# Optimization experiments

Measured on AMD Instinct MI355X. Metric: run time of the kernel, lower is better.

The kernel has to match this reference:

```python
import jax, jax.numpy as jnp
import numpy as np

KS, STRIDE, DIL = 5, 1, 1
PAD = (KS + (KS - 1) * (DIL - 1) - 1) // 2
EPS = 1e-5


def _unfold_t(x):
    # x: (N, C, T, V) -> (N, C, T_out, KS, V), zero-padded temporal windows
    N, C, T, V = x.shape
    xp = jnp.pad(x, ((0, 0), (0, 0), (PAD, PAD), (0, 0)))
    t_out = (T + 2 * PAD - DIL * (KS - 1) - 1) // STRIDE + 1
    idx = jnp.arange(t_out)[:, None] * STRIDE + jnp.arange(KS)[None, :] * DIL  # (T_out, KS)
    return xp[:, :, idx, :]


def _bn2d(x, g, b):
    # training-mode BatchNorm2d: biased batch stats over (N, T, V)
    mu = jnp.mean(x, axis=(0, 2, 3), keepdims=True)
    var = jnp.var(x, axis=(0, 2, 3), keepdims=True)
    xn = (x - mu) * jax.lax.rsqrt(var + EPS)
    return xn * g[None, :, None, None] + b[None, :, None, None]


def setup_inputs() -> dict:
    key = jax.random.key(0)
    ks = jax.random.split(key, 8)
    N, C, T, V = 64, 64, 128, 25
    R, O = 8, 128
    s = 0.05
    return {
        "x": jax.random.normal(ks[0], (N, C, T, V), jnp.float32),
        "Wv": jax.random.normal(ks[1], (R, C), jnp.float32) * s,
        "bv": jax.random.normal(ks[2], (R,), jnp.float32) * s,
        "Ww": jax.random.normal(ks[3], (KS * KS, KS), jnp.float32) * s,
        "bw": jax.random.normal(ks[4], (KS * KS,), jnp.float32) * s,
        "g_bn": jnp.ones((R,), jnp.float32),
        "b_bn": jnp.zeros((R,), jnp.float32),
        "Wr": jax.random.normal(ks[5], (R, C), jnp.float32) * s,
        "br": jax.random.normal(ks[6], (R,), jnp.float32) * s,
        "g_r": jnp.ones((R,), jnp.float32),
        "b_r": jnp.zeros((R,), jnp.float32),
        "Wo": jax.random.normal(ks[7], (O, R), jnp.float32) * s,
        "bo": jnp.zeros((O,), jnp.float32),
        "g_o": jnp.ones((O,), jnp.float32),
        "b_o": jnp.zeros((O,), jnp.float32),
    }


def reference(x, Wv, bv, Ww, bw, g_bn, b_bn, Wr, br, g_r, b_r, Wo, bo, g_o, b_o):
    N, C, T, V = x.shape
    # convV (1x1) then unfold both x and v
    v0 = jnp.einsum('rc,nctv->nrtv', Wv, x) + bv[None, :, None, None]
    xu = _unfold_t(x)      # (N, C, T, W, V)
    vu = _unfold_t(v0)     # (N, R, T, W, V)
    # mean over channels, move window dim to channel position for convW
    m = jnp.mean(xu, axis=1).transpose(0, 2, 1, 3)  # (N, W, T, V)
    w = jnp.einsum('ow,nwtv->notv', Ww, m) + bw[None, :, None, None]
    weights = jnp.tanh(w.reshape(N, KS, KS, T, V))  # (N, W, W, T, V)
    att = jnp.einsum('nwutv,nctuv->nctv', weights, vu)  # (N, R, T, V)
    # residual 1x1 conv + BN (in_channels != out_channels -> conv path)
    res = _bn2d(jnp.einsum('rc,nctv->nrtv', Wr, x) + br[None, :, None, None], g_r, b_r)
    h = _bn2d(att, g_bn, b_bn) + res
    h = jnp.where(h >= 0, h, 0.1 * h)  # LeakyReLU(0.1)
    out = _bn2d(jnp.einsum('or,nrtv->notv', Wo, h) + bo[None, :, None, None], g_o, b_o)
    return out
```

## Files before the change

### kernel.cpp

```cpp
#include <hip/hip_runtime.h>
#include <math.h>

#define TV 3200
#define NTV 204800
#define NB1 512
#define NB2 400
constexpr float EPSF = 1e-5f;

typedef float f2 __attribute__((ext_vector_type(2)));

__device__ inline float fast_tanh(float x){
  float e = __expf(2.f*x);
  return 1.f - 2.f/(e + 1.f);
}

template<int NS>
__device__ inline void write_partials4(float (&vals)[NS], float* __restrict__ outp, int nb, float* lds){
  __syncthreads();
  int lane = threadIdx.x & 63, wid = threadIdx.x >> 6;
  #pragma unroll
  for (int s = 0; s < NS; ++s){
    float v = vals[s];
    #pragma unroll
    for (int o = 32; o > 0; o >>= 1) v += __shfl_down(v, o);
    if (lane == 0) lds[s*4 + wid] = v;
  }
  __syncthreads();
  if ((int)threadIdx.x < NS)
    outp[threadIdx.x*nb + blockIdx.x] = lds[threadIdx.x*4+0] + lds[threadIdx.x*4+1]
                                      + lds[threadIdx.x*4+2] + lds[threadIdx.x*4+3];
}

__global__ __launch_bounds__(256) void k_pw(
    const float* __restrict__ x,
    const float* __restrict__ Wv, const float* __restrict__ bv,
    const float* __restrict__ Wr, const float* __restrict__ br,
    const float* __restrict__ Ww, const float* __restrict__ bw,
    float* __restrict__ r0, float* __restrict__ att,
    float* __restrict__ pr, float* __restrict__ patt)
{
  __shared__ float sV[500*9];
  __shared__ float sS[500];
  __shared__ float sWv[512], sWr[512], sWw[125], sbw[25];
  __shared__ float red[16*4];
  const int tid = threadIdx.x;
  const int b = blockIdx.x, n = b >> 3, q = b & 7;
  const int t0 = q*16;
  for (int i2 = tid; i2 < 512; i2 += 256){ sWv[i2] = Wv[i2]; sWr[i2] = Wr[i2]; }
  if (tid < 125) sWw[tid] = Ww[tid];
  if (tid < 25)  sbw[tid] = bw[tid];
  __syncthreads();

  const int i = tid;
  const bool act = (i < 250);
  const int s0 = 2*i, s1 = 2*i + 1;
  const bool val0 = act && (q > 0 || s0 >= 50) && (q < 7 || s0 < 450);
  const bool val1 = act && (q > 0 || s1 >= 50) && (q < 7 || s1 < 450);
  const bool own  = (i >= 25) && (i < 225);
  const float* xpn = x + (size_t)n*64*TV + (t0*25 - 50);

  float av0[8]={0,0,0,0,0,0,0,0}, av1[8]={0,0,0,0,0,0,0,0};
  float ar0[8]={0,0,0,0,0,0,0,0}, ar1[8]={0,0,0,0,0,0,0,0};
  float ss0 = 0.f, ss1 = 0.f;
  if (val0 && val1){
    #pragma unroll 8
    for (int c = 0; c < 64; ++c){
      f2 xv = *(const f2*)(xpn + (size_t)c*TV + s0);
      ss0 += xv.x; ss1 += xv.y;
      #pragma unroll
      for (int r = 0; r < 8; ++r){
        float wv = sWv[r*64+c], wr = sWr[r*64+c];
        av0[r] = fmaf(wv, xv.x, av0[r]); av1[r] = fmaf(wv, xv.y, av1[r]);
        ar0[r] = fmaf(wr, xv.x, ar0[r]); ar1[r] = fmaf(wr, xv.y, ar1[r]);
      }
    }
  } else if (val0 || val1){
    #pragma unroll 4
    for (int c = 0; c < 64; ++c){
      float x0 = 0.f, x1 = 0.f;
      if (val0) x0 = xpn[(size_t)c*TV + s0];
      if (val1) x1 = xpn[(size_t)c*TV + s1];
      ss0 += x0; ss1 += x1;
      #pragma unroll
      for (int r = 0; r < 8; ++r){
        float wv = sWv[r*64+c], wr = sWr[r*64+c];
        av0[r] = fmaf(wv, x0, av0[r]); av1[r] = fmaf(wv, x1, av1[r]);
        ar0[r] = fmaf(wr, x0, ar0[r]); ar1[r] = fmaf(wr, x1, ar1[r]);
      }
    }
  }
  if (act){
    sS[s0] = ss0 * 0.015625f;
    sS[s1] = ss1 * 0.015625f;
    #pragma unroll
    for (int r = 0; r < 8; ++r){
      float bvr = bv[r];
      sV[s0*9+r] = val0 ? (av0[r] + bvr) : 0.f;
      sV[s1*9+r] = val1 ? (av1[r] + bvr) : 0.f;
    }
  }
  const int gbase = t0*25 - 50 + s0;
  float vals[16];
  {
    float rr0[8], rr1[8];
    if (own){
      float* rp = r0 + (size_t)n*8*TV + gbase;
      #pragma unroll
      for (int r = 0; r < 8; ++r){
        float brr = br[r];
        rr0[r] = ar0[r] + brr; rr1[r] = ar1[r] + brr;
        f2 rv; rv.x = rr0[r]; rv.y = rr1[r];
        *(f2*)(rp + (size_t)r*TV) = rv;
      }
    }
    #pragma unroll
    for (int r = 0; r < 8; ++r){
      vals[r]   = own ? (rr0[r] + rr1[r]) : 0.f;
      vals[8+r] = own ? (rr0[r]*rr0[r] + rr1[r]*rr1[r]) : 0.f;
    }
  }
  write_partials4<16>(vals, pr, NB1, red);

  float at0[8]={0,0,0,0,0,0,0,0}, at1[8]={0,0,0,0,0,0,0,0};
  if (own){
    #pragma unroll
    for (int sl = 0; sl < 2; ++sl){
      int s = s0 + sl;
      float m[5];
      #pragma unroll
      for (int k = 0; k < 5; ++k) m[k] = sS[s + (k-2)*25];
      float w2[5] = {0.f,0.f,0.f,0.f,0.f};
      #pragma unroll
      for (int w = 0; w < 5; ++w){
        #pragma unroll
        for (int u = 0; u < 5; ++u){
          int o = w*5 + u;
          float wo = sbw[o];
          #pragma unroll
          for (int k = 0; k < 5; ++k) wo = fmaf(sWw[o*5+k], m[k], wo);
          w2[u] += fast_tanh(wo);
        }
      }
      float* at = sl ? at1 : at0;
      #pragma unroll
      for (int u = 0; u < 5; ++u){
        float wu = w2[u];
        int base = (s + (u-2)*25)*9;
        #pragma unroll
        for (int r = 0; r < 8; ++r) at[r] = fmaf(wu, sV[base + r], at[r]);
      }
    }
    float* ap = att + (size_t)n*8*TV + gbase;
    #pragma unroll
    for (int r = 0; r < 8; ++r){
      f2 av; av.x = at0[r]; av.y = at1[r];
      *(f2*)(ap + (size_t)r*TV) = av;
    }
  }
  #pragma unroll
  for (int r = 0; r < 8; ++r){
    vals[r]   = own ? (at0[r] + at1[r]) : 0.f;
    vals[8+r] = own ? (at0[r]*at0[r] + at1[r]*at1[r]) : 0.f;
  }
  write_partials4<16>(vals, patt, NB1, red);
}

__global__ __launch_bounds__(256) void k_h(
    const float* __restrict__ att, const float* __restrict__ r0,
    const float* __restrict__ pr, const float* __restrict__ patt,
    const float* __restrict__ g_bn, const float* __restrict__ b_bn,
    const float* __restrict__ g_r, const float* __restrict__ b_r,
    float* __restrict__ h, float* __restrict__ ph)
{
  __shared__ float red[44*4];
  __shared__ float sc[32];
  const int tid = threadIdx.x;
  {
    int g = tid >> 3, l8 = tid & 7;
    const float* src = (g < 16) ? (pr + g*NB1) : (patt + (g-16)*NB1);
    float sm = 0.f;
    for (int k2 = l8; k2 < NB1; k2 += 8) sm += src[k2];
    sm += __shfl_down(sm, 4, 8); sm += __shfl_down(sm, 2, 8); sm += __shfl_down(sm, 1, 8);
    if (l8 == 0) red[g] = sm;
  }
  __syncthreads();
  if (tid < 8){
    int r = tid;
    float mu_r  = red[r]    / (float)NTV;
    float var_r = red[8+r]  / (float)NTV - mu_r*mu_r;
    float ar_ = g_r[r] * rsqrtf(var_r + EPSF);
    sc[16+r] = ar_; sc[24+r] = b_r[r] - ar_*mu_r;
    float mu_a  = red[16+r] / (float)NTV;
    float var_a = red[24+r] / (float)NTV - mu_a*mu_a;
    float aa = g_bn[r] * rsqrtf(var_a + EPSF);
    sc[r] = aa; sc[8+r] = b_bn[r] - aa*mu_a;
  }
  __syncthreads();

  int p = blockIdx.x*256 + tid;
  int n = p / 1600, j = p - n*1600;
  const float* ap = att + (size_t)n*8*TV + 2*j;
  const float* rp = r0  + (size_t)n*8*TV + 2*j;
  float* hp = h + (size_t)n*8*TV + 2*j;
  float h0[8], h1[8];
  #pragma unroll
  for (int r = 0; r < 8; ++r){
    float ca = sc[r], cc = sc[8+r], cr = sc[16+r], cd = sc[24+r];
    f2 a = *(const f2*)(ap + (size_t)r*TV);
    f2 rr = *(const f2*)(rp + (size_t)r*TV);
    float z0 = ca*a.x + cc + cr*rr.x + cd;
    float z1 = ca*a.y + cc + cr*rr.y + cd;
    h0[r] = (z0 >= 0.f) ? z0 : 0.1f*z0;
    h1[r] = (z1 >= 0.f) ? z1 : 0.1f*z1;
    f2 hh; hh.x = h0[r]; hh.y = h1[r];
    *(f2*)(hp + (size_t)r*TV) = hh;
  }
  float vals[44];
  #pragma unroll
  for (int r = 0; r < 8; ++r) vals[r] = h0[r] + h1[r];
  int cnt = 8;
  #pragma unroll
  for (int r = 0; r < 8; ++r){
    #pragma unroll
    for (int r2 = r; r2 < 8; ++r2) vals[cnt++] = h0[r]*h0[r2] + h1[r]*h1[r2];
  }
  write_partials4<44>(vals, ph, NB2, red);
}

__global__ __launch_bounds__(256) void k_out(
    const float* __restrict__ h, const float* __restrict__ ph,
    const float* __restrict__ Wo, const float* __restrict__ bo,
    const float* __restrict__ g_o, const float* __restrict__ b_o,
    float* __restrict__ out)
{
  __shared__ float hstat[44];
  __shared__ float sW[1024], sB[128];
  const int tid = threadIdx.x;
  {
    int lane = tid & 63, wid = tid >> 6;
    for (int s2 = wid; s2 < 44; s2 += 4){
      float sm = 0.f;
      for (int k2 = lane; k2 < NB2; k2 += 64) sm += ph[s2*NB2 + k2];
      #pragma unroll
      for (int o = 32; o > 0; o >>= 1) sm += __shfl_down(sm, o);
      if (lane == 0) hstat[s2] = sm;
    }
  }
  __syncthreads();
  if (tid < 128){
    int o = tid;
    double muh[8];
    #pragma unroll
    for (int r = 0; r < 8; ++r) muh[r] = (double)hstat[r] / (double)NTV;
    double w[8];
    #pragma unroll
    for (int r = 0; r < 8; ++r) w[r] = (double)Wo[o*8+r];
    double bob = (double)bo[o];
    double mu = bob;
    #pragma unroll
    for (int r = 0; r < 8; ++r) mu += w[r]*muh[r];
    double t = 0.0;
    for (int r = 0; r < 8; ++r){
      for (int r2 = 0; r2 < 8; ++r2){
        int lo = (r < r2) ? r : r2, hi = (r < r2) ? r2 : r;
        int idx = 8 + lo*8 - (lo*(lo-1))/2 + (hi - lo);
        t += w[r]*w[r2]*((double)hstat[idx] / (double)NTV);
      }
    }
    double ey2 = t + 2.0*bob*(mu - bob) + bob*bob;
    double var = ey2 - mu*mu;
    double a = (double)g_o[o] / sqrt(var + (double)EPSF);
    #pragma unroll
    for (int r = 0; r < 8; ++r) sW[o*8+r] = (float)(a * w[r]);
    sB[o] = (float)(a * (bob - mu) + (double)b_o[o]);
  }
  __syncthreads();

  int p = blockIdx.x*256 + tid;
  int n = p / 1600, j = p - n*1600;
  const float* hp = h + (size_t)n*8*TV + 2*j;
  float h0[8], h1[8];
  #pragma unroll
  for (int r = 0; r < 8; ++r){
    f2 v = *(const f2*)(hp + (size_t)r*TV);
    h0[r] = v.x; h1[r] = v.y;
  }
  float* op = out + (size_t)n*128*TV + 2*j;
  #pragma unroll 8
  for (int o = 0; o < 128; ++o){
    float y0 = sB[o], y1 = y0;
    #pragma unroll
    for (int r = 0; r < 8; ++r){
      float w = sW[o*8+r];
      y0 = fmaf(w, h0[r], y0); y1 = fmaf(w, h1[r], y1);
    }
    f2 yy; yy.x = y0; yy.y = y1;
    __builtin_nontemporal_store(yy, (f2*)(op + (size_t)o*TV));
  }
}

extern "C" void kernel_launch(void* const* d_in, const int* in_sizes, int n_in,
                              void* d_out, int out_size, void* d_ws, size_t ws_size,
                              hipStream_t stream){
  const float* x    = (const float*)d_in[0];
  const float* Wv   = (const float*)d_in[1];
  const float* bv   = (const float*)d_in[2];
  const float* Ww   = (const float*)d_in[3];
  const float* bw   = (const float*)d_in[4];
  const float* g_bn = (const float*)d_in[5];
  const float* b_bn = (const float*)d_in[6];
  const float* Wr   = (const float*)d_in[7];
  const float* br   = (const float*)d_in[8];
  const float* g_r  = (const float*)d_in[9];
  const float* b_r  = (const float*)d_in[10];
  const float* Wo   = (const float*)d_in[11];
  const float* bo   = (const float*)d_in[12];
  const float* g_o  = (const float*)d_in[13];
  const float* b_o  = (const float*)d_in[14];

  float* ws = (float*)d_ws;
  size_t off = 0;
  float* r0   = ws + off; off += 1638400;
  float* att  = ws + off; off += 1638400;
  float* hbuf = ws + off; off += 1638400;
  float* pr   = ws + off; off += 16*NB1;
  float* patt = ws + off; off += 16*NB1;
  float* ph   = ws + off; off += 44*NB2;

  k_pw <<<NB1, 256, 0, stream>>>(x, Wv, bv, Wr, br, Ww, bw, r0, att, pr, patt);
  k_h  <<<NB2, 256, 0, stream>>>(att, r0, pr, patt, g_bn, b_bn, g_r, b_r, hbuf, ph);
  k_out<<<NB2, 256, 0, stream>>>(hbuf, ph, Wo, bo, g_o, b_o, (float*)d_out);
}
```

Measured before the change: 234.0 us.

## Widen k_h/k_out to 4 elements per thread and transpose pointwise weights

k_h and k_out now use 128-thread blocks, and each thread handles 4 contiguous positions with float4 loads and stores instead of 2 with float2. The partial-sum reductions are adapted for two waves. In k_pw the Wv/Wr weights are stored transposed in shared memory so they can be read as float4, the two loop variants are merged into one, and x is read with nontemporal loads. The goal is fewer memory instructions and LDS reads per element. The cost is higher register pressure per thread and fewer threads per block in the latency-sensitive phases.

```diff
diff --git a/kernel.cpp b/kernel.cpp
--- a/kernel.cpp
+++ b/kernel.cpp
@@ -4,10 +4,11 @@
 #define TV 3200
 #define NTV 204800
 #define NB1 512
-#define NB2 400
+#define NBH 400
 constexpr float EPSF = 1e-5f;
 
 typedef float f2 __attribute__((ext_vector_type(2)));
+typedef float f4 __attribute__((ext_vector_type(4)));
 
 __device__ inline float fast_tanh(float x){
   float e = __expf(2.f*x);
@@ -29,6 +30,22 @@
   if ((int)threadIdx.x < NS)
     outp[threadIdx.x*nb + blockIdx.x] = lds[threadIdx.x*4+0] + lds[threadIdx.x*4+1]
                                       + lds[threadIdx.x*4+2] + lds[threadIdx.x*4+3];
+}
+
+template<int NS>
+__device__ inline void write_partials2(float (&vals)[NS], float* __restrict__ outp, int nb, float* lds){
+  __syncthreads();
+  int lane = threadIdx.x & 63, wid = threadIdx.x >> 6;
+  #pragma unroll
+  for (int s = 0; s < NS; ++s){
+    float v = vals[s];
+    #pragma unroll
+    for (int o = 32; o > 0; o >>= 1) v += __shfl_down(v, o);
+    if (lane == 0) lds[s*2 + wid] = v;
+  }
+  __syncthreads();
+  if ((int)threadIdx.x < NS)
+    outp[threadIdx.x*nb + blockIdx.x] = lds[threadIdx.x*2+0] + lds[threadIdx.x*2+1];
 }
 
 __global__ __launch_bounds__(256) void k_pw(
@@ -41,12 +58,17 @@
 {
   __shared__ float sV[500*9];
   __shared__ float sS[500];
-  __shared__ float sWv[512], sWr[512], sWw[125], sbw[25];
+  __shared__ float sWvT[512], sWrT[512];
+  __shared__ float sWw[125], sbw[25];
   __shared__ float red[16*4];
   const int tid = threadIdx.x;
   const int b = blockIdx.x, n = b >> 3, q = b & 7;
   const int t0 = q*16;
-  for (int i2 = tid; i2 < 512; i2 += 256){ sWv[i2] = Wv[i2]; sWr[i2] = Wr[i2]; }
+  for (int i2 = tid; i2 < 512; i2 += 256){
+    int c = i2 >> 3, r = i2 & 7;
+    sWvT[i2] = Wv[r*64 + c];
+    sWrT[i2] = Wr[r*64 + c];
+  }
   if (tid < 125) sWw[tid] = Ww[tid];
   if (tid < 25)  sbw[tid] = bw[tid];
   __syncthreads();
@@ -58,35 +80,31 @@
   const bool val1 = act && (q > 0 || s1 >= 50) && (q < 7 || s1 < 450);
   const bool own  = (i >= 25) && (i < 225);
   const float* xpn = x + (size_t)n*64*TV + (t0*25 - 50);
+  const f4* sWvT4 = (const f4*)sWvT;
+  const f4* sWrT4 = (const f4*)sWrT;
 
   float av0[8]={0,0,0,0,0,0,0,0}, av1[8]={0,0,0,0,0,0,0,0};
   float ar0[8]={0,0,0,0,0,0,0,0}, ar1[8]={0,0,0,0,0,0,0,0};
   float ss0 = 0.f, ss1 = 0.f;
-  if (val0 && val1){
-    #pragma unroll 8
-    for (int c = 0; c < 64; ++c){
-      f2 xv = *(const f2*)(xpn + (size_t)c*TV + s0);
-      ss0 += xv.x; ss1 += xv.y;
-      #pragma unroll
-      for (int r = 0; r < 8; ++r){
-        float wv = sWv[r*64+c], wr = sWr[r*64+c];
-        av0[r] = fmaf(wv, xv.x, av0[r]); av1[r] = fmaf(wv, xv.y, av1[r]);
-        ar0[r] = fmaf(wr, xv.x, ar0[r]); ar1[r] = fmaf(wr, xv.y, ar1[r]);
-      }
-    }
-  } else if (val0 || val1){
-    #pragma unroll 4
-    for (int c = 0; c < 64; ++c){
-      float x0 = 0.f, x1 = 0.f;
+  #pragma unroll 4
+  for (int c = 0; c < 64; ++c){
+    float x0 = 0.f, x1 = 0.f;
+    if (val0 && val1){
+      f2 xv = __builtin_nontemporal_load((const f2*)(xpn + (size_t)c*TV + s0));
+      x0 = xv.x; x1 = xv.y;
+    } else {
       if (val0) x0 = xpn[(size_t)c*TV + s0];
       if (val1) x1 = xpn[(size_t)c*TV + s1];
-      ss0 += x0; ss1 += x1;
-      #pragma unroll
-      for (int r = 0; r < 8; ++r){
-        float wv = sWv[r*64+c], wr = sWr[r*64+c];
-        av0[r] = fmaf(wv, x0, av0[r]); av1[r] = fmaf(wv, x1, av1[r]);
-        ar0[r] = fmaf(wr, x0, ar0[r]); ar1[r] = fmaf(wr, x1, ar1[r]);
-      }
+    }
+    ss0 += x0; ss1 += x1;
+    f4 wv0 = sWvT4[c*2], wv1 = sWvT4[c*2+1];
+    f4 wr0 = sWrT4[c*2], wr1 = sWrT4[c*2+1];
+    #pragma unroll
+    for (int r = 0; r < 4; ++r){
+      av0[r]   = fmaf(wv0[r], x0, av0[r]);   av1[r]   = fmaf(wv0[r], x1, av1[r]);
+      ar0[r]   = fmaf(wr0[r], x0, ar0[r]);   ar1[r]   = fmaf(wr0[r], x1, ar1[r]);
+      av0[4+r] = fmaf(wv1[r], x0, av0[4+r]); av1[4+r] = fmaf(wv1[r], x1, av1[4+r]);
+      ar0[4+r] = fmaf(wr1[r], x0, ar0[4+r]); ar1[4+r] = fmaf(wr1[r], x1, ar1[4+r]);
     }
   }
   if (act){
@@ -165,23 +183,23 @@
   write_partials4<16>(vals, patt, NB1, red);
 }
 
-__global__ __launch_bounds__(256) void k_h(
+__global__ __launch_bounds__(128) void k_h(
     const float* __restrict__ att, const float* __restrict__ r0,
     const float* __restrict__ pr, const float* __restrict__ patt,
     const float* __restrict__ g_bn, const float* __restrict__ b_bn,
     const float* __restrict__ g_r, const float* __restrict__ b_r,
     float* __restrict__ h, float* __restrict__ ph)
 {
-  __shared__ float red[44*4];
+  __shared__ float red[44*2];
   __shared__ float sc[32];
   const int tid = threadIdx.x;
   {
-    int g = tid >> 3, l8 = tid & 7;
+    int g = tid >> 2, l4 = tid & 3;
     const float* src = (g < 16) ? (pr + g*NB1) : (patt + (g-16)*NB1);
     float sm = 0.f;
-    for (int k2 = l8; k2 < NB1; k2 += 8) sm += src[k2];
-    sm += __shfl_down(sm, 4, 8); sm += __shfl_down(sm, 2, 8); sm += __shfl_down(sm, 1, 8);
-    if (l8 == 0) red[g] = sm;
+    for (int k2 = l4; k2 < NB1; k2 += 4) sm += src[k2];
+    sm += __shfl_down(sm, 2, 4); sm += __shfl_down(sm, 1, 4);
+    if (l4 == 0) red[g] = sm;
   }
   __syncthreads();
   if (tid < 8){
@@ -197,37 +215,41 @@
   }
   __syncthreads();
 
-  int p = blockIdx.x*256 + tid;
-  int n = p / 1600, j = p - n*1600;
-  const float* ap = att + (size_t)n*8*TV + 2*j;
-  const float* rp = r0  + (size_t)n*8*TV + 2*j;
-  float* hp = h + (size_t)n*8*TV + 2*j;
-  float h0[8], h1[8];
+  int p = blockIdx.x*128 + tid;
+  int n = p / 800, j = p - n*800;
+  const float* ap = att + (size_t)n*8*TV + 4*j;
+  const float* rp = r0  + (size_t)n*8*TV + 4*j;
+  float* hp = h + (size_t)n*8*TV + 4*j;
+  float hh[8][4];
   #pragma unroll
   for (int r = 0; r < 8; ++r){
-    float ca = sc[r], cc = sc[8+r], cr = sc[16+r], cd = sc[24+r];
-    f2 a = *(const f2*)(ap + (size_t)r*TV);
-    f2 rr = *(const f2*)(rp + (size_t)r*TV);
-    float z0 = ca*a.x + cc + cr*rr.x + cd;
-    float z1 = ca*a.y + cc + cr*rr.y + cd;
-    h0[r] = (z0 >= 0.f) ? z0 : 0.1f*z0;
-    h1[r] = (z1 >= 0.f) ? z1 : 0.1f*z1;
-    f2 hh; hh.x = h0[r]; hh.y = h1[r];
-    *(f2*)(hp + (size_t)r*TV) = hh;
+    float ca = sc[r], cc = sc[8+r] + sc[24+r], cr = sc[16+r];
+    f4 a  = *(const f4*)(ap + (size_t)r*TV);
+    f4 rr = *(const f4*)(rp + (size_t)r*TV);
+    f4 hv;
+    #pragma unroll
+    for (int e = 0; e < 4; ++e){
+      float z = fmaf(ca, a[e], fmaf(cr, rr[e], cc));
+      hh[r][e] = (z >= 0.f) ? z : 0.1f*z;
+      hv[e] = hh[r][e];
+    }
+    *(f4*)(hp + (size_t)r*TV) = hv;
   }
   float vals[44];
   #pragma unroll
-  for (int r = 0; r < 8; ++r) vals[r] = h0[r] + h1[r];
+  for (int r = 0; r < 8; ++r) vals[r] = hh[r][0]+hh[r][1]+hh[r][2]+hh[r][3];
   int cnt = 8;
   #pragma unroll
   for (int r = 0; r < 8; ++r){
     #pragma unroll
-    for (int r2 = r; r2 < 8; ++r2) vals[cnt++] = h0[r]*h0[r2] + h1[r]*h1[r2];
-  }
-  write_partials4<44>(vals, ph, NB2, red);
-}
-
-__global__ __launch_bounds__(256) void k_out(
+    for (int r2 = r; r2 < 8; ++r2)
+      vals[cnt++] = hh[r][0]*hh[r2][0] + hh[r][1]*hh[r2][1]
+                  + hh[r][2]*hh[r2][2] + hh[r][3]*hh[r2][3];
+  }
+  write_partials2<44>(vals, ph, NBH, red);
+}
+
+__global__ __launch_bounds__(128) void k_out(
     const float* __restrict__ h, const float* __restrict__ ph,
     const float* __restrict__ Wo, const float* __restrict__ bo,
     const float* __restrict__ g_o, const float* __restrict__ b_o,
@@ -238,16 +260,16 @@
   const int tid = threadIdx.x;
   {
     int lane = tid & 63, wid = tid >> 6;
-    for (int s2 = wid; s2 < 44; s2 += 4){
+    for (int s2 = wid; s2 < 44; s2 += 2){
       float sm = 0.f;
-      for (int k2 = lane; k2 < NB2; k2 += 64) sm += ph[s2*NB2 + k2];
+      for (int k2 = lane; k2 < NBH; k2 += 64) sm += ph[s2*NBH + k2];
       #pragma unroll
       for (int o = 32; o > 0; o >>= 1) sm += __shfl_down(sm, o);
       if (lane == 0) hstat[s2] = sm;
     }
   }
   __syncthreads();
-  if (tid < 128){
+  {
     int o = tid;
     double muh[8];
     #pragma unroll
@@ -276,26 +298,31 @@
   }
   __syncthreads();
 
-  int p = blockIdx.x*256 + tid;
-  int n = p / 1600, j = p - n*1600;
-  const float* hp = h + (size_t)n*8*TV + 2*j;
-  float h0[8], h1[8];
+  int p = blockIdx.x*128 + tid;
+  int n = p / 800, j = p - n*800;
+  const float* hp = h + (size_t)n*8*TV + 4*j;
+  float hh[8][4];
   #pragma unroll
   for (int r = 0; r < 8; ++r){
-    f2 v = *(const f2*)(hp + (size_t)r*TV);
-    h0[r] = v.x; h1[r] = v.y;
-  }
-  float* op = out + (size_t)n*128*TV + 2*j;
-  #pragma unroll 8
+    f4 v = *(const f4*)(hp + (size_t)r*TV);
+    hh[r][0] = v[0]; hh[r][1] = v[1]; hh[r][2] = v[2]; hh[r][3] = v[3];
+  }
+  const f4* sW4 = (const f4*)sW;
+  float* op = out + (size_t)n*128*TV + 4*j;
+  #pragma unroll 4
   for (int o = 0; o < 128; ++o){
-    float y0 = sB[o], y1 = y0;
-    #pragma unroll
-    for (int r = 0; r < 8; ++r){
-      float w = sW[o*8+r];
-      y0 = fmaf(w, h0[r], y0); y1 = fmaf(w, h1[r], y1);
-    }
-    f2 yy; yy.x = y0; yy.y = y1;
-    __builtin_nontemporal_store(yy, (f2*)(op + (size_t)o*TV));
+    f4 w0 = sW4[o*2], w1 = sW4[o*2+1];
+    float b = sB[o];
+    f4 y; y.x = b; y.y = b; y.z = b; y.w = b;
+    #pragma unroll
+    for (int r = 0; r < 4; ++r){
+      #pragma unroll
+      for (int e = 0; e < 4; ++e){
+        y[e] = fmaf(w0[r], hh[r][e], y[e]);
+        y[e] = fmaf(w1[r], hh[4+r][e], y[e]);
+      }
+    }
+    __builtin_nontemporal_store(y, (f4*)(op + (size_t)o*TV));
   }
 }
 
@@ -325,9 +352,9 @@
   float* hbuf = ws + off; off += 1638400;
   float* pr   = ws + off; off += 16*NB1;
   float* patt = ws + off; off += 16*NB1;
-  float* ph   = ws + off; off += 44*NB2;
+  float* ph   = ws + off; off += 44*NBH;
 
   k_pw <<<NB1, 256, 0, stream>>>(x, Wv, bv, Wr, br, Ww, bw, r0, att, pr, patt);
-  k_h  <<<NB2, 256, 0, stream>>>(att, r0, pr, patt, g_bn, b_bn, g_r, b_r, hbuf, ph);
-  k_out<<<NB2, 256, 0, stream>>>(hbuf, ph, Wo, bo, g_o, b_o, (float*)d_out);
-}
+  k_h  <<<NBH, 128, 0, stream>>>(att, r0, pr, patt, g_bn, b_bn, g_r, b_r, hbuf, ph);
+  k_out<<<NBH, 128, 0, stream>>>(hbuf, ph, Wo, bo, g_o, b_o, (float*)d_out);
+}
```

Measured after the change: 269.3 us. 15.0% more time.
